# Optimization experiments

Hardware: AMD Instinct MI355X
Metric: run time of the kernel (lower is better)

## Reference

```python
import jax, jax.numpy as jnp
import numpy as np

N_NODES = 100000
N_EDGES = 1600000
N_FEAT, N_HID, N_CLS = 256, 64, 16


def setup_inputs() -> dict:
    key = jax.random.key(0)
    ks = jax.random.split(key, 8)
    x = jax.random.normal(ks[0], (N_NODES, N_FEAT), dtype=jnp.float32)
    adj_row = jax.random.randint(ks[1], (N_EDGES,), 0, N_NODES, dtype=jnp.int32)
    adj_col = jax.random.randint(ks[2], (N_EDGES,), 0, N_NODES, dtype=jnp.int32)
    adj_vals = jax.random.uniform(ks[3], (N_EDGES,), dtype=jnp.float32)
    W1 = jax.random.normal(ks[4], (N_FEAT, N_HID), dtype=jnp.float32) * 0.05
    b1 = jnp.zeros((N_HID,), dtype=jnp.float32)
    W2 = jax.random.normal(ks[5], (N_HID, N_CLS), dtype=jnp.float32) * 0.05
    b2 = jnp.zeros((N_CLS,), dtype=jnp.float32)
    return {"x": x, "adj_row": adj_row, "adj_col": adj_col, "adj_vals": adj_vals,
            "W1": W1, "b1": b1, "W2": W2, "b2": b2}


def _spmm(row, col, vals, h):
    # sparse [N,N] @ dense [N,D]: gather source rows, scale, scatter-add to dest rows
    msgs = vals[:, None] * h[col]                       # [E, D]
    return jax.ops.segment_sum(msgs, row, num_segments=N_NODES)


def reference(x, adj_row, adj_col, adj_vals, W1, b1, W2, b2):
    # layer 1: linear -> spmm -> relu  (dropout is identity at inference)
    h = _spmm(adj_row, adj_col, adj_vals, x @ W1 + b1)  # [N, n_hidden]
    h = jax.nn.relu(h)
    # layer 2: linear -> spmm -> log_softmax
    out = _spmm(adj_row, adj_col, adj_vals, h @ W2 + b2)  # [N, n_class]
    return jax.nn.log_softmax(out, axis=1)
```

## Files before the change

### kernel.cpp

```cpp
#include <hip/hip_runtime.h>

#define N_NODES 100000
#define N_EDGES 1600000
#define N_FEAT  256
#define N_HID   64
#define N_CLS   16
#define NB      391
#define CHUNK   8192

typedef unsigned short bfraw;
typedef unsigned int uint32;

typedef __attribute__((ext_vector_type(8))) short  bf16x8;
typedef __attribute__((ext_vector_type(4))) float  f32x4;

__device__ __forceinline__ bfraw f2bf(float f) {
    union { float f; unsigned int i; } v; v.f = f;
    unsigned int x = v.i;
    return (bfraw)((x + 0x7FFFu + ((x >> 16) & 1u)) >> 16);
}

__device__ __forceinline__ float bf_lo(uint32 g) { return __uint_as_float(g << 16); }
__device__ __forceinline__ float bf_hi(uint32 g) { return __uint_as_float(g & 0xFFFF0000u); }

__global__ __launch_bounds__(256) void w1cvt_hist_k(const float* __restrict__ W1,
                                                    bfraw* __restrict__ w1f,
                                                    const int* __restrict__ rowi,
                                                    int* __restrict__ bcnt) {
    __shared__ int lh[NB];
    if (blockIdx.x < 64) {
        int i = blockIdx.x * 256 + threadIdx.x;
        int k = i >> 6, n = i & 63;
        w1f[((size_t)((k >> 3) * 64 + n) << 3) + (k & 7)] = f2bf(W1[i]);
        return;
    }
    for (int i = threadIdx.x; i < NB; i += 256) lh[i] = 0;
    __syncthreads();
    for (int e = (blockIdx.x - 64) * 256 + threadIdx.x; e < N_EDGES; e += 256 * 256)
        atomicAdd(&lh[rowi[e] >> 8], 1);
    __syncthreads();
    for (int i = threadIdx.x; i < NB; i += 256) {
        int c = lh[i];
        if (c) atomicAdd(&bcnt[i], c);
    }
}

__global__ __launch_bounds__(256) void gemm1_k(const float* __restrict__ x,
                                               const bfraw* __restrict__ w1f,
                                               const float* __restrict__ b1,
                                               bfraw* __restrict__ h0) {
    const int t    = threadIdx.x;
    const int w    = t >> 6;
    const int lane = t & 63;
    const int q    = lane >> 4;
    const int m    = lane & 15;

    const int row  = blockIdx.x * 64 + w * 16 + m;
    const int srow = row < N_NODES ? row : N_NODES - 1;
    const float* xp = x + (size_t)srow * N_FEAT + q * 8;
    const bf16x8* w1v = (const bf16x8*)w1f;

    f32x4 acc[4];
    #pragma unroll
    for (int nt = 0; nt < 4; ++nt) acc[nt] = (f32x4){0.f, 0.f, 0.f, 0.f};

    #pragma unroll
    for (int s = 0; s < 8; ++s) {
        float4 a0 = *(const float4*)(xp + s * 32);
        float4 a1 = *(const float4*)(xp + s * 32 + 4);
        bf16x8 af;
        af[0] = (short)f2bf(a0.x); af[1] = (short)f2bf(a0.y);
        af[2] = (short)f2bf(a0.z); af[3] = (short)f2bf(a0.w);
        af[4] = (short)f2bf(a1.x); af[5] = (short)f2bf(a1.y);
        af[6] = (short)f2bf(a1.z); af[7] = (short)f2bf(a1.w);
        const int g = s * 4 + q;
        #pragma unroll
        for (int nt = 0; nt < 4; ++nt) {
            bf16x8 bf_ = w1v[g * 64 + nt * 16 + m];
            acc[nt] = __builtin_amdgcn_mfma_f32_16x16x32_bf16(af, bf_, acc[nt], 0, 0, 0);
        }
    }

    float bb[4];
    #pragma unroll
    for (int nt = 0; nt < 4; ++nt) bb[nt] = b1[nt * 16 + m];

    const int orow0 = blockIdx.x * 64 + w * 16 + q * 4;
    #pragma unroll
    for (int r = 0; r < 4; ++r) {
        int orow = orow0 + r;
        if (orow < N_NODES) {
            bfraw* op = h0 + (size_t)orow * N_HID + m;
            #pragma unroll
            for (int nt = 0; nt < 4; ++nt)
                op[nt * 16] = f2bf(acc[nt][r] + bb[nt]);
        }
    }
}

__global__ __launch_bounds__(512) void bscan_k(const int* __restrict__ bcnt,
                                               int* __restrict__ bbase,
                                               int* __restrict__ gcur,
                                               int* __restrict__ rp) {
    __shared__ int s[512];
    int t = threadIdx.x;
    int v = (t < NB) ? bcnt[t] : 0;
    s[t] = v;
    __syncthreads();
    #pragma unroll
    for (int off = 1; off < 512; off <<= 1) {
        int x = (t >= off) ? s[t - off] : 0;
        __syncthreads();
        s[t] += x;
        __syncthreads();
    }
    if (t <= NB) {
        int b = s[t] - v;
        bbase[t] = b;
        if (t < NB) gcur[t] = b;
    }
    if (t == 0) rp[N_NODES] = N_EDGES;
}

__global__ __launch_bounds__(256) void scatter_k(const int* __restrict__ rowi,
                                                 const int* __restrict__ coli,
                                                 const float* __restrict__ vals,
                                                 int* __restrict__ gcur,
                                                 int2* __restrict__ edges) {
    __shared__ int lh[NB];
    __shared__ int lb[NB];
    const int t  = threadIdx.x;
    const int e0 = blockIdx.x * CHUNK;
    for (int i = t; i < NB; i += 256) lh[i] = 0;
    __syncthreads();
    for (int j = t; j < CHUNK; j += 256) {
        int e = e0 + j;
        if (e < N_EDGES) atomicAdd(&lh[rowi[e] >> 8], 1);
    }
    __syncthreads();
    for (int i = t; i < NB; i += 256) {
        int c = lh[i];
        lb[i] = c ? atomicAdd(&gcur[i], c) : 0;
        lh[i] = 0;
    }
    __syncthreads();
    for (int j = t; j < CHUNK; j += 256) {
        int e = e0 + j;
        if (e < N_EDGES) {
            int r  = rowi[e];
            int b  = r >> 8;
            int rk = atomicAdd(&lh[b], 1);
            edges[lb[b] + rk] = make_int2(coli[e] | ((r & 255) << 17),
                                          __float_as_int(vals[e]));
        }
    }
}

__global__ __launch_bounds__(256) void sort_k(const int* __restrict__ bbase,
                                              const int2* __restrict__ edges,
                                              int2* __restrict__ edges2,
                                              int* __restrict__ rp) {
    __shared__ int cnt[256];
    __shared__ int pos[256];
    const int t   = threadIdx.x;
    const int b   = blockIdx.x;
    const int beg = bbase[b];
    const int end = bbase[b + 1];

    cnt[t] = 0;
    __syncthreads();
    for (int i = beg + t; i < end; i += 256)
        atomicAdd(&cnt[(edges[i].x >> 17) & 255], 1);
    __syncthreads();

    int v = cnt[t];
    pos[t] = v;
    __syncthreads();
    #pragma unroll
    for (int off = 1; off < 256; off <<= 1) {
        int y = (t >= off) ? pos[t - off] : 0;
        __syncthreads();
        pos[t] += y;
        __syncthreads();
    }
    int excl = pos[t] - v;

    int row = (b << 8) + t;
    if (row < N_NODES) rp[row] = beg + excl;
    __syncthreads();
    pos[t] = excl;
    __syncthreads();

    for (int i = beg + t; i < end; i += 256) {
        int2 E = edges[i];
        int r  = (E.x >> 17) & 255;
        int rk = atomicAdd(&pos[r], 1);
        edges2[beg + rk] = make_int2(E.x & 0x1FFFF, E.y);
    }
}

__global__ __launch_bounds__(256) void spmm1_fused3_k(const int* __restrict__ rp,
                                                      const int2* __restrict__ edges2,
                                                      const uint32* __restrict__ h0p,
                                                      const float* __restrict__ W2,
                                                      const float* __restrict__ b2,
                                                      float* __restrict__ h2) {
    __shared__ float Hs[16][68];
    __shared__ float Ws[64 * 16];
    __shared__ float bs[16];
    const int t = threadIdx.x;
    *(float4*)&Ws[t * 4] = ((const float4*)W2)[t];
    if (t < 16) bs[t] = b2[t];

    const int g16 = t >> 4;
    const int l   = t & 15;
    const int row = blockIdx.x * 16 + g16;
    const int beg = rp[row];
    const int end = rp[row + 1];

    const uint2* h0v = (const uint2*)h0p;

    float a0 = 0.f, a1 = 0.f, a2 = 0.f, a3 = 0.f;
    int i = beg;
    for (; i + 8 <= end; i += 8) {
        int2 E[8];
        #pragma unroll
        for (int u = 0; u < 8; ++u) E[u] = edges2[i + u];
        uint2 q[8];
        #pragma unroll
        for (int u = 0; u < 8; ++u) q[u] = h0v[(size_t)E[u].x * 16 + l];
        #pragma unroll
        for (int u = 0; u < 8; ++u) {
            float v = __int_as_float(E[u].y);
            a0 += v * bf_lo(q[u].x); a1 += v * bf_hi(q[u].x);
            a2 += v * bf_lo(q[u].y); a3 += v * bf_hi(q[u].y);
        }
    }
    for (; i + 4 <= end; i += 4) {
        int2 E[4];
        #pragma unroll
        for (int u = 0; u < 4; ++u) E[u] = edges2[i + u];
        uint2 q[4];
        #pragma unroll
        for (int u = 0; u < 4; ++u) q[u] = h0v[(size_t)E[u].x * 16 + l];
        #pragma unroll
        for (int u = 0; u < 4; ++u) {
            float v = __int_as_float(E[u].y);
            a0 += v * bf_lo(q[u].x); a1 += v * bf_hi(q[u].x);
            a2 += v * bf_lo(q[u].y); a3 += v * bf_hi(q[u].y);
        }
    }
    for (; i < end; ++i) {
        int2 E = edges2[i];
        uint2 q = h0v[(size_t)E.x * 16 + l];
        float v = __int_as_float(E.y);
        a0 += v * bf_lo(q.x); a1 += v * bf_hi(q.x);
        a2 += v * bf_lo(q.y); a3 += v * bf_hi(q.y);
    }

    *(float4*)&Hs[g16][4 * l] = make_float4(fmaxf(a0, 0.f), fmaxf(a1, 0.f),
                                            fmaxf(a2, 0.f), fmaxf(a3, 0.f));
    __syncthreads();

    const int r = t >> 4;
    const int c = t & 15;
    float a = bs[c];
    #pragma unroll
    for (int k = 0; k < 64; ++k)
        a += Hs[r][k] * Ws[k * 16 + c];
    h2[(size_t)(blockIdx.x * 16 + r) * N_CLS + c] = a;
}

__global__ __launch_bounds__(256) void spmm2_lsm_k(const int* __restrict__ rp,
                                                   const int2* __restrict__ edges2,
                                                   const float* __restrict__ h2,
                                                   float* __restrict__ outp) {
    const int l   = threadIdx.x & 7;
    const int row = blockIdx.x * 32 + (threadIdx.x >> 3);
    const int beg = rp[row];
    const int end = rp[row + 1];
    const float2* h2v = (const float2*)h2;

    float a0 = 0.f, a1 = 0.f;
    int i = beg;
    for (; i + 4 <= end; i += 4) {
        int2 e0 = edges2[i + 0], e1 = edges2[i + 1];
        int2 e2 = edges2[i + 2], e3 = edges2[i + 3];
        float2 g0 = h2v[(size_t)e0.x * 8 + l];
        float2 g1 = h2v[(size_t)e1.x * 8 + l];
        float2 g2 = h2v[(size_t)e2.x * 8 + l];
        float2 g3 = h2v[(size_t)e3.x * 8 + l];
        float v0 = __int_as_float(e0.y), v1 = __int_as_float(e1.y);
        float v2 = __int_as_float(e2.y), v3 = __int_as_float(e3.y);
        a0 += v0 * g0.x; a1 += v0 * g0.y;
        a0 += v1 * g1.x; a1 += v1 * g1.y;
        a0 += v2 * g2.x; a1 += v2 * g2.y;
        a0 += v3 * g3.x; a1 += v3 * g3.y;
    }
    for (; i < end; ++i) {
        int2 e = edges2[i];
        float2 g = h2v[(size_t)e.x * 8 + l];
        float v = __int_as_float(e.y);
        a0 += v * g.x; a1 += v * g.y;
    }

    float m = fmaxf(a0, a1);
    #pragma unroll
    for (int off = 4; off; off >>= 1) m = fmaxf(m, __shfl_xor(m, off, 8));
    float ex = expf(a0 - m) + expf(a1 - m);
    float s = ex;
    #pragma unroll
    for (int off = 4; off; off >>= 1) s += __shfl_xor(s, off, 8);
    float ls = logf(s);
    *(float2*)(outp + (size_t)row * N_CLS + 2 * l) =
        make_float2(a0 - m - ls, a1 - m - ls);
}

extern "C" void kernel_launch(void* const* d_in, const int* in_sizes, int n_in,
                              void* d_out, int out_size, void* d_ws, size_t ws_size,
                              hipStream_t stream) {
    const float* x        = (const float*)d_in[0];
    const int*   adj_row  = (const int*)d_in[1];
    const int*   adj_col  = (const int*)d_in[2];
    const float* adj_vals = (const float*)d_in[3];
    const float* W1       = (const float*)d_in[4];
    const float* b1       = (const float*)d_in[5];
    const float* W2       = (const float*)d_in[6];
    const float* b2       = (const float*)d_in[7];
    float*       out      = (float*)d_out;

    const size_t H0_BYTES = (size_t)N_NODES * N_HID * sizeof(bfraw);
    const size_t H2_BYTES = (size_t)N_NODES * N_CLS * sizeof(float);
    const size_t E_BYTES  = (size_t)N_EDGES * sizeof(int2);
    bfraw* h0     = (bfraw*)d_ws;
    float* h2     = (float*)((char*)d_ws + H0_BYTES);
    int2*  edges  = (int2*)((char*)h2 + H2_BYTES);
    int2*  edges2 = (int2*)((char*)edges + E_BYTES);
    int*   bcnt   = (int*)((char*)edges2 + E_BYTES);
    int*   bbase  = bcnt + NB;
    int*   gcur   = bbase + NB + 1;
    int*   rp     = gcur + NB;
    bfraw* w1f    = (bfraw*)(rp + N_NODES + 1);

    hipMemsetAsync(bcnt, 0, NB * sizeof(int), stream);
    w1cvt_hist_k<<<320, 256, 0, stream>>>(W1, w1f, adj_row, bcnt);
    bscan_k<<<1, 512, 0, stream>>>(bcnt, bbase, gcur, rp);
    scatter_k<<<(N_EDGES + CHUNK - 1) / CHUNK, 256, 0, stream>>>(adj_row, adj_col,
                                                                 adj_vals, gcur, edges);
    sort_k<<<NB, 256, 0, stream>>>(bbase, edges, edges2, rp);

    gemm1_k<<<(N_NODES + 63) / 64, 256, 0, stream>>>(x, w1f, b1, h0);
    spmm1_fused3_k<<<N_NODES / 16, 256, 0, stream>>>(rp, edges2, (const uint32*)h0,
                                                     W2, b2, h2);

    spmm2_lsm_k<<<N_NODES / 32, 256, 0, stream>>>(rp, edges2, h2, out);
}
```

Before: 328.0 us.

## Fuse CSR build stages into one cooperative kernel with grid syncs

Replaces the memset, histogram, scan, scatter and per-bucket sort kernels with a single cooperative kernel of 1024 blocks that uses grid-wide syncs between phases. Each block's per-bucket histogram stays in shared memory from the counting phase through the scatter phase, so the row indices are read once less. The scan is redone as a single-wavefront shuffle scan. The goal is to remove launch gaps and the extra pass over the edges, at the cost of four grid barriers and a dependence on all blocks being co-resident.

New measurement: 737.8 us. 2.25x slower.

```diff
diff --git a/kernel.cpp b/kernel.cpp
--- a/kernel.cpp
+++ b/kernel.cpp
@@ -1,4 +1,7 @@
 #include <hip/hip_runtime.h>
+#include <hip/hip_cooperative_groups.h>
+
+namespace cg = cooperative_groups;
 
 #define N_NODES 100000
 #define N_EDGES 1600000
@@ -6,7 +9,8 @@
 #define N_HID   64
 #define N_CLS   16
 #define NB      391
-#define CHUNK   8192
+#define GRID_B  1024
+#define CHUNK2  1568
 
 typedef unsigned short bfraw;
 typedef unsigned int uint32;
@@ -23,25 +27,122 @@
 __device__ __forceinline__ float bf_lo(uint32 g) { return __uint_as_float(g << 16); }
 __device__ __forceinline__ float bf_hi(uint32 g) { return __uint_as_float(g & 0xFFFF0000u); }
 
-__global__ __launch_bounds__(256) void w1cvt_hist_k(const float* __restrict__ W1,
-                                                    bfraw* __restrict__ w1f,
-                                                    const int* __restrict__ rowi,
-                                                    int* __restrict__ bcnt) {
+__global__ __launch_bounds__(256) void build_k(const float* __restrict__ W1,
+                                               bfraw* __restrict__ w1f,
+                                               const int* __restrict__ rowi,
+                                               const int* __restrict__ coli,
+                                               const float* __restrict__ vals,
+                                               int* __restrict__ bcnt,
+                                               int* __restrict__ bbase,
+                                               int* __restrict__ gcur,
+                                               int* __restrict__ rp,
+                                               int2* __restrict__ edges,
+                                               int2* __restrict__ edges2) {
+    cg::grid_group grid = cg::this_grid();
     __shared__ int lh[NB];
-    if (blockIdx.x < 64) {
-        int i = blockIdx.x * 256 + threadIdx.x;
+    __shared__ int lb[NB];
+    const int t  = threadIdx.x;
+    const int b  = blockIdx.x;
+    const int e0 = b * CHUNK2;
+
+    if (b == 0)
+        for (int i = t; i < NB; i += 256) bcnt[i] = 0;
+    if (b < 64) {
+        int i = b * 256 + t;
         int k = i >> 6, n = i & 63;
         w1f[((size_t)((k >> 3) * 64 + n) << 3) + (k & 7)] = f2bf(W1[i]);
-        return;
-    }
-    for (int i = threadIdx.x; i < NB; i += 256) lh[i] = 0;
+    }
+    for (int i = t; i < NB; i += 256) lh[i] = 0;
     __syncthreads();
-    for (int e = (blockIdx.x - 64) * 256 + threadIdx.x; e < N_EDGES; e += 256 * 256)
-        atomicAdd(&lh[rowi[e] >> 8], 1);
-    __syncthreads();
-    for (int i = threadIdx.x; i < NB; i += 256) {
+    for (int j = t; j < CHUNK2; j += 256) {
+        int e = e0 + j;
+        if (e < N_EDGES) atomicAdd(&lh[rowi[e] >> 8], 1);
+    }
+    grid.sync();
+
+    for (int i = t; i < NB; i += 256) {
         int c = lh[i];
         if (c) atomicAdd(&bcnt[i], c);
+    }
+    grid.sync();
+
+    if (b == 0 && t < 64) {
+        int carry = 0;
+        #pragma unroll
+        for (int tile = 0; tile < 7; ++tile) {
+            int idx = tile * 64 + t;
+            int v = (idx < NB) ? bcnt[idx] : 0;
+            int inc = v;
+            #pragma unroll
+            for (int off = 1; off < 64; off <<= 1) {
+                int y = __shfl_up(inc, off);
+                if (t >= off) inc += y;
+            }
+            if (idx < NB) {
+                int excl = carry + inc - v;
+                bbase[idx] = excl;
+                gcur[idx]  = excl;
+            }
+            carry += __shfl(inc, 63);
+        }
+        if (t == 0) { bbase[NB] = N_EDGES; rp[N_NODES] = N_EDGES; }
+    }
+    grid.sync();
+
+    for (int i = t; i < NB; i += 256) {
+        int c = lh[i];
+        lb[i] = c ? atomicAdd(&gcur[i], c) : 0;
+        lh[i] = 0;
+    }
+    __syncthreads();
+    for (int j = t; j < CHUNK2; j += 256) {
+        int e = e0 + j;
+        if (e < N_EDGES) {
+            int r  = rowi[e];
+            int bk = r >> 8;
+            int rk = atomicAdd(&lh[bk], 1);
+            edges[lb[bk] + rk] = make_int2(coli[e] | ((r & 255) << 17),
+                                           __float_as_int(vals[e]));
+        }
+    }
+    grid.sync();
+
+    if (b < NB) {
+        int* cnt = lh;
+        int* pos = lb;
+        const int beg = bbase[b];
+        const int end = bbase[b + 1];
+
+        cnt[t] = 0;
+        __syncthreads();
+        for (int i = beg + t; i < end; i += 256)
+            atomicAdd(&cnt[(edges[i].x >> 17) & 255], 1);
+        __syncthreads();
+
+        int v = cnt[t];
+        pos[t] = v;
+        __syncthreads();
+        #pragma unroll
+        for (int off = 1; off < 256; off <<= 1) {
+            int y = (t >= off) ? pos[t - off] : 0;
+            __syncthreads();
+            pos[t] += y;
+            __syncthreads();
+        }
+        int excl = pos[t] - v;
+
+        int row = (b << 8) + t;
+        if (row < N_NODES) rp[row] = beg + excl;
+        __syncthreads();
+        pos[t] = excl;
+        __syncthreads();
+
+        for (int i = beg + t; i < end; i += 256) {
+            int2 E = edges[i];
+            int r  = (E.x >> 17) & 255;
+            int rk = atomicAdd(&pos[r], 1);
+            edges2[beg + rk] = make_int2(E.x & 0x1FFFF, E.y);
+        }
     }
 }
 
@@ -95,107 +196,6 @@
             for (int nt = 0; nt < 4; ++nt)
                 op[nt * 16] = f2bf(acc[nt][r] + bb[nt]);
         }
-    }
-}
-
-__global__ __launch_bounds__(512) void bscan_k(const int* __restrict__ bcnt,
-                                               int* __restrict__ bbase,
-                                               int* __restrict__ gcur,
-                                               int* __restrict__ rp) {
-    __shared__ int s[512];
-    int t = threadIdx.x;
-    int v = (t < NB) ? bcnt[t] : 0;
-    s[t] = v;
-    __syncthreads();
-    #pragma unroll
-    for (int off = 1; off < 512; off <<= 1) {
-        int x = (t >= off) ? s[t - off] : 0;
-        __syncthreads();
-        s[t] += x;
-        __syncthreads();
-    }
-    if (t <= NB) {
-        int b = s[t] - v;
-        bbase[t] = b;
-        if (t < NB) gcur[t] = b;
-    }
-    if (t == 0) rp[N_NODES] = N_EDGES;
-}
-
-__global__ __launch_bounds__(256) void scatter_k(const int* __restrict__ rowi,
-                                                 const int* __restrict__ coli,
-                                                 const float* __restrict__ vals,
-                                                 int* __restrict__ gcur,
-                                                 int2* __restrict__ edges) {
-    __shared__ int lh[NB];
-    __shared__ int lb[NB];
-    const int t  = threadIdx.x;
-    const int e0 = blockIdx.x * CHUNK;
-    for (int i = t; i < NB; i += 256) lh[i] = 0;
-    __syncthreads();
-    for (int j = t; j < CHUNK; j += 256) {
-        int e = e0 + j;
-        if (e < N_EDGES) atomicAdd(&lh[rowi[e] >> 8], 1);
-    }
-    __syncthreads();
-    for (int i = t; i < NB; i += 256) {
-        int c = lh[i];
-        lb[i] = c ? atomicAdd(&gcur[i], c) : 0;
-        lh[i] = 0;
-    }
-    __syncthreads();
-    for (int j = t; j < CHUNK; j += 256) {
-        int e = e0 + j;
-        if (e < N_EDGES) {
-            int r  = rowi[e];
-            int b  = r >> 8;
-            int rk = atomicAdd(&lh[b], 1);
-            edges[lb[b] + rk] = make_int2(coli[e] | ((r & 255) << 17),
-                                          __float_as_int(vals[e]));
-        }
-    }
-}
-
-__global__ __launch_bounds__(256) void sort_k(const int* __restrict__ bbase,
-                                              const int2* __restrict__ edges,
-                                              int2* __restrict__ edges2,
-                                              int* __restrict__ rp) {
-    __shared__ int cnt[256];
-    __shared__ int pos[256];
-    const int t   = threadIdx.x;
-    const int b   = blockIdx.x;
-    const int beg = bbase[b];
-    const int end = bbase[b + 1];
-
-    cnt[t] = 0;
-    __syncthreads();
-    for (int i = beg + t; i < end; i += 256)
-        atomicAdd(&cnt[(edges[i].x >> 17) & 255], 1);
-    __syncthreads();
-
-    int v = cnt[t];
-    pos[t] = v;
-    __syncthreads();
-    #pragma unroll
-    for (int off = 1; off < 256; off <<= 1) {
-        int y = (t >= off) ? pos[t - off] : 0;
-        __syncthreads();
-        pos[t] += y;
-        __syncthreads();
-    }
-    int excl = pos[t] - v;
-
-    int row = (b << 8) + t;
-    if (row < N_NODES) rp[row] = beg + excl;
-    __syncthreads();
-    pos[t] = excl;
-    __syncthreads();
-
-    for (int i = beg + t; i < end; i += 256) {
-        int2 E = edges[i];
-        int r  = (E.x >> 17) & 255;
-        int rk = atomicAdd(&pos[r], 1);
-        edges2[beg + rk] = make_int2(E.x & 0x1FFFF, E.y);
     }
 }
 
@@ -342,12 +342,10 @@
     int*   rp     = gcur + NB;
     bfraw* w1f    = (bfraw*)(rp + N_NODES + 1);
 
-    hipMemsetAsync(bcnt, 0, NB * sizeof(int), stream);
-    w1cvt_hist_k<<<320, 256, 0, stream>>>(W1, w1f, adj_row, bcnt);
-    bscan_k<<<1, 512, 0, stream>>>(bcnt, bbase, gcur, rp);
-    scatter_k<<<(N_EDGES + CHUNK - 1) / CHUNK, 256, 0, stream>>>(adj_row, adj_col,
-                                                                 adj_vals, gcur, edges);
-    sort_k<<<NB, 256, 0, stream>>>(bbase, edges, edges2, rp);
+    void* bargs[] = {(void*)&W1, (void*)&w1f, (void*)&adj_row, (void*)&adj_col,
+                     (void*)&adj_vals, (void*)&bcnt, (void*)&bbase, (void*)&gcur,
+                     (void*)&rp, (void*)&edges, (void*)&edges2};
+    hipLaunchCooperativeKernel(build_k, dim3(GRID_B), dim3(256), bargs, 0u, stream);
 
     gemm1_k<<<(N_NODES + 63) / 64, 256, 0, stream>>>(x, w1f, b1, h0);
     spmm1_fused3_k<<<N_NODES / 16, 256, 0, stream>>>(rp, edges2, (const uint32*)h0,
```
